# Performance work log

Hardware: AMD Instinct MI355X
Metric: run time of the kernel (lower is better)

Reference implementation:

```python
import jax, jax.numpy as jnp
import numpy as np

B, T, C, L = 1024, 256, 128, 64
NEG = -1e30  # finite stand-in for -inf (safe gradients)
EPS = 1e-7   # keras.backend.epsilon()


def setup_inputs() -> dict:
    key = jax.random.key(0)
    k1, k2 = jax.random.split(key)
    # y_pred is a softmax output (probabilities), as keras ctc_batch_cost expects
    logits = jax.random.normal(k1, (B, T, C), dtype=jnp.float32)
    y_pred = jax.nn.softmax(logits, axis=-1)
    # labels in [0, C-2]; class C-1 is the CTC blank (keras convention)
    y_true = jax.random.randint(k2, (B, L), 0, C - 1, dtype=jnp.int64)
    return {"y_true": y_true, "y_pred": y_pred}


def ctc_loss(y_true, y_pred):
    """Negative log-likelihood CTC loss per sample, shape [B, 1].
    Matches keras.backend.ctc_batch_cost with full input/label lengths,
    blank index = num_classes - 1, log(y_pred + eps)."""
    Bb, Tt, Cc = y_pred.shape
    Ll = y_true.shape[1]
    blank = Cc - 1
    S = 2 * Ll + 1  # extended label: blank, l1, blank, l2, ..., blank

    logp = jnp.log(y_pred + EPS)  # [B, T, C]

    ext = jnp.full((Bb, S), blank, dtype=y_true.dtype).at[:, 1::2].set(y_true)  # [B, S]
    # per-(t, s) log-prob of the extended symbol: lp[b, t, s] = logp[b, t, ext[b, s]]
    lp = jnp.take_along_axis(logp, ext[:, None, :], axis=2)  # [B, T, S]

    # skip transition s-2 -> s allowed iff ext[s] != blank and ext[s] != ext[s-2]
    ext_m2 = jnp.concatenate(
        [jnp.full((Bb, 2), blank, dtype=ext.dtype), ext[:, :-2]], axis=1)
    can_skip = (ext != blank) & (ext != ext_m2)  # [B, S]

    def shift1(a):
        return jnp.concatenate(
            [jnp.full((Bb, 1), NEG, dtype=a.dtype), a[:, :-1]], axis=1)

    # alpha init at t=0: only s=0 (blank) and s=1 (first label) reachable
    alpha0 = (jnp.full((Bb, S), NEG, dtype=lp.dtype)
              .at[:, 0].set(lp[:, 0, 0])
              .at[:, 1].set(lp[:, 0, 1]))

    def step(alpha, lp_t):
        a1 = shift1(alpha)
        a2 = jnp.where(can_skip, shift1(shift1(alpha)), NEG)
        new = jax.nn.logsumexp(jnp.stack([alpha, a1, a2], axis=0), axis=0) + lp_t
        return new, None

    lp_tbs = jnp.swapaxes(lp, 0, 1)  # [T, B, S]
    alpha, _ = jax.lax.scan(step, alpha0, lp_tbs[1:])

    log_lik = jnp.logaddexp(alpha[:, S - 1], alpha[:, S - 2])  # end on last blank or last label
    return -log_lik[:, None]  # [B, 1], matching ctc_batch_cost output shape


def reference(y_true, y_pred):
    return ctc_loss(y_true, y_pred)
```

## Files before the change

kernel.cpp:

```cpp
#include <hip/hip_runtime.h>
#include <math.h>


#define Bn 1024
#define Tn 256
#define Cn 128
#define Ln 64
#define BLANK 127
#define U 8
#define NCH (Tn / U)
#define RING 8
#define EPS128 (1e-7f * 128.0f)
#define LN2 0.69314718055994530942f

#define WAIT_LGKM0() __builtin_amdgcn_s_waitcnt(0xC07F)

template <int CTRL>
__device__ __forceinline__ float dpp_movf(float x) {
    return __int_as_float(__builtin_amdgcn_update_dpp(
        0, __float_as_int(x), CTRL, 0xF, 0xF, true));
}
__device__ __forceinline__ int dpp_shr1_i(int x) {
    return __builtin_amdgcn_update_dpp(0, x, 0x138, 0xF, 0xF, true);
}

__global__ __launch_bounds__(256)
void ctc_pc_kernel(const int* __restrict__ yt,
                   const float* __restrict__ yp,
                   float* __restrict__ out) {
    __shared__ __align__(16) float ring[RING][U * Cn];
    __shared__ int flags[NCH];
    __shared__ int cons_prog;
    volatile int* vfl = flags;
    volatile int* vpr = &cons_prog;

    const int b = blockIdx.x;
    const int t = threadIdx.x;
    const int w = t >> 6;
    const int i = t & 63;

    if (t < NCH) flags[t] = 0;
    if (t == 0)  cons_prog = 0;
    __syncthreads();

    const float* gb = yp + (size_t)b * (Tn * Cn);

    if (w != 0) {
        const int start = w - 1;
        float4 fA[4], fB[4];
        auto issue = [&](int c, float4* f) {
            const float4* p = (const float4*)(gb + c * (U * Cn)) + i;
#pragma unroll
            for (int k = 0; k < 4; ++k) f[k] = p[k * 64];
        };
        auto put = [&](int c, const float4* f) {
            while (*vpr < c - (RING - 1)) __builtin_amdgcn_s_sleep(1);
            float4* d = (float4*)ring[c & (RING - 1)] + i;
#pragma unroll
            for (int k = 0; k < 4; ++k) d[k * 64] = f[k];
            WAIT_LGKM0();
            if (i == 0) vfl[c] = 1;
        };
        issue(start, fA);
        if (start + 3 < NCH) issue(start + 3, fB);
        for (int c = start; c < NCH; c += 6) {
            put(c, fA);
            if (c + 6 < NCH) issue(c + 6, fA);
            if (c + 3 < NCH) {
                put(c + 3, fB);
                if (c + 9 < NCH) issue(c + 9, fB);
            }
        }
        return;
    }

    const int li = yt[b * Ln + i];
    const int ll = dpp_shr1_i(li);
    const float skf = (li != ll) ? 1.0f : 0.0f;

    float qlA[U], qbA[U], qlB[U], qbB[U];
    auto spinflag = [&](int c) {
        while (vfl[c] == 0) __builtin_amdgcn_s_sleep(1);
        __builtin_amdgcn_sched_barrier(0);
    };
    auto qread = [&](int c, float* ql, float* qb) {
        const float* s = ring[c & (RING - 1)];
#pragma unroll
        for (int j = 0; j < U; ++j) {
            ql[j] = fmaf(s[j * Cn + li],    128.0f, EPS128);
            qb[j] = fmaf(s[j * Cn + BLANK], 128.0f, EPS128);
        }
    };

    float E = 0.f, O = 0.f, X = 0.f;
    int Esum = 0;

    auto steps = [&](const float* ql, const float* qb, bool first) {
#pragma unroll
        for (int j = 0; j < U; ++j) {
            if (first && j == 0) {
                E = (i == 0) ? qb[0] : 0.f;
                O = (i == 0) ? ql[0] : 0.f;
                X = 0.f;
                continue;
            }
            const float Ol = dpp_movf<0x138>(O);
            const float t1 = O + E;
            const float nO = fmaf(skf, Ol, t1) * ql[j];
            const float nE = (E + Ol) * qb[j];
            const float nX = (X + O) * qb[j];
            E = nE; O = nO; X = nX;
        }
    };
    auto renorm = [&]() {
        float m = fmaxf(E, O);
        if (i == 63) m = fmaxf(m, X);
        m = fmaxf(m, dpp_movf<0x111>(m));
        m = fmaxf(m, dpp_movf<0x112>(m));
        m = fmaxf(m, dpp_movf<0x114>(m));
        m = fmaxf(m, dpp_movf<0x118>(m));
        m = fmaxf(m, dpp_movf<0x142>(m));
        m = fmaxf(m, dpp_movf<0x143>(m));
        const unsigned ub =
            (unsigned)__builtin_amdgcn_readlane(__float_as_int(m), 63);
        const int eb = (int)(ub >> 23);
        const float sc = __int_as_float((unsigned)(254 - eb) << 23);
        Esum += eb - 127;
        E *= sc; O *= sc; X *= sc;
    };

    spinflag(0);
    qread(0, qlA, qbA);
    for (int c = 0; c < NCH - 2; c += 2) {
        spinflag(c + 1);
        qread(c + 1, qlB, qbB);
        steps(qlA, qbA, c == 0);
        renorm();
        if (i == 0) *vpr = c + 1;
        spinflag(c + 2);
        qread(c + 2, qlA, qbA);
        steps(qlB, qbB, false);
        renorm();
        if (i == 0) *vpr = c + 2;
    }
    spinflag(NCH - 1);
    qread(NCH - 1, qlB, qbB);
    steps(qlA, qbA, false);
    renorm();
    if (i == 0) *vpr = NCH - 1;
    steps(qlB, qbB, false);

    if (i == 63) {
        const float s = O + X;
#if __has_builtin(__builtin_amdgcn_logf)
        const float l2 = __builtin_amdgcn_logf(s);
#else
        const float l2 = log2f(s);
#endif
        out[b] = -(l2 + (float)(Esum - 7 * Tn)) * LN2;
    }
}

extern "C" void kernel_launch(void* const* d_in, const int* in_sizes, int n_in,
                              void* d_out, int out_size, void* d_ws, size_t ws_size,
                              hipStream_t stream) {
    const int*   y_true = (const int*)d_in[0];
    const float* y_pred = (const float*)d_in[1];
    float*       out    = (float*)d_out;
    hipLaunchKernelGGL(ctc_pc_kernel, dim3(Bn), dim3(256), 0, stream,
                       y_true, y_pred, out);
}
```

Baseline: 217.1 us.

## Replace producer-consumer ring with two-phase gather into compact bf16 LDS table

```diff
diff --git a/kernel.cpp b/kernel.cpp
--- a/kernel.cpp
+++ b/kernel.cpp
@@ -9,11 +9,9 @@
 #define BLANK 127
 #define U 8
 #define NCH (Tn / U)
-#define RING 8
+#define ENT 65
 #define EPS128 (1e-7f * 128.0f)
 #define LN2 0.69314718055994530942f
-
-#define WAIT_LGKM0() __builtin_amdgcn_s_waitcnt(0xC07F)
 
 template <int CTRL>
 __device__ __forceinline__ float dpp_movf(float x) {
@@ -23,72 +21,62 @@
 __device__ __forceinline__ int dpp_shr1_i(int x) {
     return __builtin_amdgcn_update_dpp(0, x, 0x138, 0xF, 0xF, true);
 }
+__device__ __forceinline__ unsigned short f2bf(float f) {
+    const unsigned u = __float_as_uint(f);
+    return (unsigned short)((u + 0x7FFFu + ((u >> 16) & 1u)) >> 16);
+}
 
 __global__ __launch_bounds__(256)
-void ctc_pc_kernel(const int* __restrict__ yt,
-                   const float* __restrict__ yp,
-                   float* __restrict__ out) {
-    __shared__ __align__(16) float ring[RING][U * Cn];
-    __shared__ int flags[NCH];
-    __shared__ int cons_prog;
-    volatile int* vfl = flags;
-    volatile int* vpr = &cons_prog;
+void ctc_fused_kernel(const int* __restrict__ yt,
+                      const float* __restrict__ yp,
+                      float* __restrict__ out) {
+    __shared__ unsigned short comp[NCH][U][ENT];
+    __shared__ __align__(16) float raw[2][U * Cn];
+    __shared__ int lab[Ln];
 
     const int b = blockIdx.x;
     const int t = threadIdx.x;
     const int w = t >> 6;
     const int i = t & 63;
 
-    if (t < NCH) flags[t] = 0;
-    if (t == 0)  cons_prog = 0;
+    if (t < Ln) lab[t] = yt[b * Ln + t];
+
+    const float4* gsrc = (const float4*)(yp + (size_t)b * (Tn * Cn));
+
+    float4 vA = gsrc[t];
+    float4 vB = gsrc[256 + t];
+    float4 vC = gsrc[512 + t];
+    const int j  = t >> 5;
+    const int tb = t & 31;
+
+    for (int c = 0; c < NCH; ++c) {
+        ((float4*)raw[c & 1])[t] = vA;
+        vA = vB; vB = vC;
+        if (c + 3 < NCH) vC = gsrc[(c + 3) * 256 + t];
+        __syncthreads();
+
+        const float* rw = raw[c & 1] + j * Cn;
+        const unsigned short q1 = f2bf(fmaf(rw[lab[tb]],      128.0f, EPS128));
+        const unsigned short q2 = f2bf(fmaf(rw[lab[tb + 32]], 128.0f, EPS128));
+        comp[c][j][tb]      = q1;
+        comp[c][j][tb + 32] = q2;
+        if (tb == 0)
+            comp[c][j][64] = f2bf(fmaf(rw[BLANK], 128.0f, EPS128));
+    }
     __syncthreads();
 
-    const float* gb = yp + (size_t)b * (Tn * Cn);
+    if (w != 0) return;
 
-    if (w != 0) {
-        const int start = w - 1;
-        float4 fA[4], fB[4];
-        auto issue = [&](int c, float4* f) {
-            const float4* p = (const float4*)(gb + c * (U * Cn)) + i;
-#pragma unroll
-            for (int k = 0; k < 4; ++k) f[k] = p[k * 64];
-        };
-        auto put = [&](int c, const float4* f) {
-            while (*vpr < c - (RING - 1)) __builtin_amdgcn_s_sleep(1);
-            float4* d = (float4*)ring[c & (RING - 1)] + i;
-#pragma unroll
-            for (int k = 0; k < 4; ++k) d[k * 64] = f[k];
-            WAIT_LGKM0();
-            if (i == 0) vfl[c] = 1;
-        };
-        issue(start, fA);
-        if (start + 3 < NCH) issue(start + 3, fB);
-        for (int c = start; c < NCH; c += 6) {
-            put(c, fA);
-            if (c + 6 < NCH) issue(c + 6, fA);
-            if (c + 3 < NCH) {
-                put(c + 3, fB);
-                if (c + 9 < NCH) issue(c + 9, fB);
-            }
-        }
-        return;
-    }
-
-    const int li = yt[b * Ln + i];
+    const int li = lab[i];
     const int ll = dpp_shr1_i(li);
     const float skf = (li != ll) ? 1.0f : 0.0f;
 
     float qlA[U], qbA[U], qlB[U], qbB[U];
-    auto spinflag = [&](int c) {
-        while (vfl[c] == 0) __builtin_amdgcn_s_sleep(1);
-        __builtin_amdgcn_sched_barrier(0);
-    };
     auto qread = [&](int c, float* ql, float* qb) {
-        const float* s = ring[c & (RING - 1)];
 #pragma unroll
-        for (int j = 0; j < U; ++j) {
-            ql[j] = fmaf(s[j * Cn + li],    128.0f, EPS128);
-            qb[j] = fmaf(s[j * Cn + BLANK], 128.0f, EPS128);
+        for (int jj = 0; jj < U; ++jj) {
+            ql[jj] = __uint_as_float((unsigned)comp[c][jj][i]  << 16);
+            qb[jj] = __uint_as_float((unsigned)comp[c][jj][64] << 16);
         }
     };
 
@@ -97,8 +85,8 @@
 
     auto steps = [&](const float* ql, const float* qb, bool first) {
 #pragma unroll
-        for (int j = 0; j < U; ++j) {
-            if (first && j == 0) {
+        for (int jj = 0; jj < U; ++jj) {
+            if (first && jj == 0) {
                 E = (i == 0) ? qb[0] : 0.f;
                 O = (i == 0) ? ql[0] : 0.f;
                 X = 0.f;
@@ -106,9 +94,9 @@
             }
             const float Ol = dpp_movf<0x138>(O);
             const float t1 = O + E;
-            const float nO = fmaf(skf, Ol, t1) * ql[j];
-            const float nE = (E + Ol) * qb[j];
-            const float nX = (X + O) * qb[j];
+            const float nO = fmaf(skf, Ol, t1) * ql[jj];
+            const float nE = (E + Ol) * qb[jj];
+            const float nX = (X + O) * qb[jj];
             E = nE; O = nO; X = nX;
         }
     };
@@ -129,25 +117,18 @@
         E *= sc; O *= sc; X *= sc;
     };
 
-    spinflag(0);
     qread(0, qlA, qbA);
     for (int c = 0; c < NCH - 2; c += 2) {
-        spinflag(c + 1);
         qread(c + 1, qlB, qbB);
         steps(qlA, qbA, c == 0);
         renorm();
-        if (i == 0) *vpr = c + 1;
-        spinflag(c + 2);
         qread(c + 2, qlA, qbA);
         steps(qlB, qbB, false);
         renorm();
-        if (i == 0) *vpr = c + 2;
     }
-    spinflag(NCH - 1);
     qread(NCH - 1, qlB, qbB);
     steps(qlA, qbA, false);
     renorm();
-    if (i == 0) *vpr = NCH - 1;
     steps(qlB, qbB, false);
 
     if (i == 63) {
@@ -167,6 +148,6 @@
     const int*   y_true = (const int*)d_in[0];
     const float* y_pred = (const float*)d_in[1];
     float*       out    = (float*)d_out;
-    hipLaunchKernelGGL(ctc_pc_kernel, dim3(Bn), dim3(256), 0, stream,
+    hipLaunchKernelGGL(ctc_fused_kernel, dim3(Bn), dim3(256), 0, stream,
                        y_true, y_pred, out);
 }
```

Measured after the change: 205.5 us. 1.06x faster.
